# Kernel tuning notes

Hardware: AMD Instinct MI355X
Metric: run time of the kernel (lower is better)

Reference implementation:

```python
import jax, jax.numpy as jnp
import numpy as np

B, N, D, H, P = 4, 512, 256, 8, 3
HD = D // H
EPS = 1e-5

def _ln(x, g, b):
    m = jnp.mean(x, axis=-1, keepdims=True)
    v = jnp.var(x, axis=-1, keepdims=True)
    return (x - m) * jax.lax.rsqrt(v + EPS) * g + b

def setup_inputs() -> dict:
    key = jax.random.key(0)
    ks = jax.random.split(key, 12)
    s = lambda *sh: 1.0 / np.sqrt(sh[0])
    return {
        "x": jax.random.normal(ks[0], (B, N, D), jnp.float32),
        "mask": jax.random.randint(ks[1], (B, N), 0, 2).astype(bool),
        "pair_feat": jax.random.normal(ks[2], (B, N, N, P), jnp.float32),
        "Wqkv": jax.random.normal(ks[3], (D, 3 * D), jnp.float32) * s(D),
        "Wout": jax.random.normal(ks[4], (D, D), jnp.float32) * s(D),
        "bout": jnp.zeros((D,), jnp.float32),
        "Wp1": jax.random.normal(ks[5], (P, D), jnp.float32) * s(P),
        "bp1": jnp.zeros((D,), jnp.float32),
        "Wp2": jax.random.normal(ks[6], (D, H), jnp.float32) * s(D),
        "bp2": jnp.zeros((H,), jnp.float32),
        "Wf1": jax.random.normal(ks[7], (D, 4 * D), jnp.float32) * s(D),
        "bf1": jnp.zeros((4 * D,), jnp.float32),
        "Wf2": jax.random.normal(ks[8], (4 * D, D), jnp.float32) * s(4 * D),
        "bf2": jnp.zeros((D,), jnp.float32),
        "g1": jnp.ones((D,), jnp.float32), "b1": jnp.zeros((D,), jnp.float32),
        "g2": jnp.ones((D,), jnp.float32), "b2": jnp.zeros((D,), jnp.float32),
    }

def reference(x, mask, pair_feat, Wqkv, Wout, bout, Wp1, bp1, Wp2, bp2,
              Wf1, bf1, Wf2, bf2, g1, b1, g2, b2):
    b_, n_, d_ = x.shape
    scale = HD ** -0.5
    qkv = x @ Wqkv                                  # [B,N,3D]
    q, k, v = jnp.split(qkv, 3, axis=-1)
    q = q.reshape(b_, n_, H, HD)
    k = k.reshape(b_, n_, H, HD)
    v = v.reshape(b_, n_, H, HD)
    logits = jnp.einsum('bihd,bjhd->bhij', q, k) * scale
    # pairwise bias MLP -> per-head bias [B,H,N,N]
    bias = jax.nn.relu(pair_feat @ Wp1 + bp1) @ Wp2 + bp2   # [B,N,N,H]
    logits = logits + jnp.transpose(bias, (0, 3, 1, 2))
    key_mask = ~mask[:, None, None, :]               # [B,1,1,N]
    logits = jnp.where(key_mask, -1e9, logits)
    attn = jax.nn.softmax(logits, axis=-1)
    out = jnp.einsum('bhij,bjhd->bihd', attn, v).reshape(b_, n_, d_)
    out = out @ Wout + bout
    x = _ln(x + out, g1, b1)
    h = jax.nn.gelu(x @ Wf1 + bf1, approximate=False) @ Wf2 + bf2
    return _ln(x + h, g2, b2)
```

## Files before the change

kernel.cpp:

```cpp
#include <hip/hip_runtime.h>
#include <hip/hip_fp16.h>
#include <math.h>

typedef unsigned short u16;
typedef short s16x8 __attribute__((ext_vector_type(8)));
typedef _Float16 f16x8 __attribute__((ext_vector_type(8)));
typedef float f32x4 __attribute__((ext_vector_type(4)));
typedef unsigned int u32x2 __attribute__((ext_vector_type(2)));

constexpr int CB = 4, CN = 512, CD = 256, CH = 8, CHD = 32;
constexpr float CEPS = 1e-5f;
constexpr int M_ROWS = CB * CN;
constexpr float QSCALE = 0.17677669529663687f;

constexpr size_t O_XB    = 0;
constexpr size_t O_QB    = 1048576;
constexpr size_t O_KB    = 2097152;
constexpr size_t O_VT    = 3145728;
constexpr size_t O_WQKVT = 4194304;
constexpr size_t O_WOUTT = O_WQKVT + 393216;
constexpr size_t O_WF1T  = O_WOUTT + 131072;
constexpr size_t O_WF2T  = O_WF1T + 524288;
constexpr size_t O_WP2T  = O_WF2T + 524288;
constexpr size_t O_PACKED= O_WP2T + 8192;
constexpr size_t O_MASKD = O_PACKED + 4096;
constexpr size_t O_BIAS  = O_MASKD + 8192;
constexpr size_t O_AOUT  = O_BIAS + 16777216;
constexpr size_t O_X1F   = O_AOUT + 1048576;
constexpr size_t O_X1B   = O_X1F + 2097152;
constexpr size_t O_H1B   = O_X1B + 1048576;
constexpr size_t O_PRE1  = O_H1B + 4194304;
constexpr size_t O_PRE2  = O_PRE1 + 2097152;

__device__ inline u16 f2b(float f) {
  union { float f; unsigned u; } v{f};
  return (u16)((v.u + 0x7FFFu + ((v.u >> 16) & 1u)) >> 16);
}
__device__ inline float b2f(u16 b) {
  union { unsigned u; float f; } v{(unsigned)b << 16};
  return v.f;
}
__device__ inline f32x4 MFMA(s16x8 a, s16x8 b, f32x4 c) {
  return __builtin_amdgcn_mfma_f32_16x16x32_bf16(a, b, c, 0, 0, 0);
}
__device__ inline f32x4 MFMAH(f16x8 a, f16x8 b, f32x4 c) {
  return __builtin_amdgcn_mfma_f32_16x16x32_f16(a, b, c, 0, 0, 0);
}
__device__ inline unsigned cvtpk(float lo, float hi) {
  unsigned r;
  asm("v_cvt_pk_bf16_f32 %0, %1, %2" : "=v"(r) : "v"(lo), "v"(hi));
  return r;
}
__device__ inline unsigned pkmax0(unsigned a) {
  unsigned d;
  asm("v_pk_max_f16 %0, %1, 0" : "=v"(d) : "v"(a));
  return d;
}

__global__ __launch_bounds__(256) void prep_kernel(
    const float* __restrict__ x, const float* __restrict__ Wqkv,
    const float* __restrict__ Wout, const float* __restrict__ Wf1,
    const float* __restrict__ Wf2, const float* __restrict__ Wp2,
    const float* __restrict__ Wp1, const float* __restrict__ bp1,
    const unsigned char* __restrict__ maskraw,
    u16* __restrict__ xb, u16* __restrict__ wqkvt, u16* __restrict__ woutt,
    u16* __restrict__ wf1t, u16* __restrict__ wf2t, u16* __restrict__ wp2t,
    unsigned* __restrict__ packed, int* __restrict__ maskd) {
  __shared__ int mode_max;
  int blk = blockIdx.x, tid = threadIdx.x;
  if (blk < 256) {
    for (int t = tid; t < 512; t += 256) {
      float4 v = ((const float4*)x)[blk * 512 + t];
      u16 o0 = f2b(v.x), o1 = f2b(v.y), o2 = f2b(v.z), o3 = f2b(v.w);
      u32x2 w; w.x = (unsigned)o0 | ((unsigned)o1 << 16);
      w.y = (unsigned)o2 | ((unsigned)o3 << 16);
      *(u32x2*)(xb + (size_t)(blk * 512 + t) * 4) = w;
    }
  } else if (blk < 352) {
    int o0 = (blk - 256) * 2048;
    for (int t = tid; t < 2048; t += 256) {
      int o = o0 + t, n = o >> 8, k = o & 255;
      wqkvt[o] = f2b(Wqkv[k * 768 + n]);
    }
  } else if (blk < 384) {
    int o0 = (blk - 352) * 2048;
    for (int t = tid; t < 2048; t += 256) {
      int o = o0 + t, n = o >> 8, k = o & 255;
      woutt[o] = f2b(Wout[k * 256 + n]);
    }
  } else if (blk < 512) {
    int o0 = (blk - 384) * 2048;
    for (int t = tid; t < 2048; t += 256) {
      int o = o0 + t, n = o >> 8, k = o & 255;
      wf1t[o] = f2b(Wf1[k * 1024 + n]);
    }
  } else if (blk < 640) {
    int o0 = (blk - 512) * 2048;
    for (int t = tid; t < 2048; t += 256) {
      int o = o0 + t, n = o >> 10, k = o & 1023;
      wf2t[o] = f2b(Wf2[k * 256 + n]);
    }
  } else if (blk == 640) {
    for (int t = tid; t < 4096; t += 256) {
      int h = t >> 8, c = t & 255;
      wp2t[t] = (h < 8) ? __half_as_ushort(__float2half(Wp2[c * 8 + h])) : (u16)0;
    }
    if (tid < 128) {
      int p = tid * 2;
      unsigned w0 = (unsigned)__half_as_ushort(__float2half(Wp1[p]))
                  | ((unsigned)__half_as_ushort(__float2half(Wp1[p + 1])) << 16);
      unsigned w1 = (unsigned)__half_as_ushort(__float2half(Wp1[256 + p]))
                  | ((unsigned)__half_as_ushort(__float2half(Wp1[256 + p + 1])) << 16);
      unsigned w2 = (unsigned)__half_as_ushort(__float2half(Wp1[512 + p]))
                  | ((unsigned)__half_as_ushort(__float2half(Wp1[512 + p + 1])) << 16);
      unsigned bb = (unsigned)__half_as_ushort(__float2half(bp1[p]))
                  | ((unsigned)__half_as_ushort(__float2half(bp1[p + 1])) << 16);
      uint4 o; o.x = w0; o.y = w1; o.z = w2; o.w = bb;
      ((uint4*)packed)[tid] = o;
    }
  } else {
    if (tid == 0) mode_max = 0;
    __syncthreads();
    int lm = 0;
    for (int i = tid; i < CB*CN; i += 256)
      if ((i & 3) != 0) lm = max(lm, (int)maskraw[i]);
    atomicMax(&mode_max, lm);
    __syncthreads();
    int mv = mode_max;
    for (int i = tid; i < CB*CN; i += 256) {
      int val;
      if (mv == 0)      val = (((const int*)maskraw)[i] != 0);
      else if (mv == 1) val = (maskraw[i] != 0);
      else              val = (((const unsigned int*)maskraw)[i] != 0);
      maskd[i] = val;
    }
  }
}

template<int EPI, int BM>
__global__ __launch_bounds__(256) void mgemm(
    const u16* __restrict__ A, const u16* __restrict__ Wt,
    const float* __restrict__ bias, const float* __restrict__ R,
    float* __restrict__ outf, u16* __restrict__ outb,
    u16* __restrict__ qb, u16* __restrict__ kb, u16* __restrict__ vt,
    int M, int N, int K) {
  constexpr int MF = BM / 32;
  __shared__ u16 As[BM * 64];
  __shared__ u16 Bs[64 * 64];
  const int tid = threadIdx.x;
  const int lane = tid & 63, w = tid >> 6;
  const int wm = w >> 1, wn = w & 1;
  const int bm = blockIdx.y * BM, bn = blockIdx.x * 64;
  f32x4 fz = {0.f, 0.f, 0.f, 0.f};
  f32x4 acc[MF][2];
#pragma unroll
  for (int mf = 0; mf < MF; ++mf) { acc[mf][0] = fz; acc[mf][1] = fz; }
  for (int k0 = 0; k0 < K; k0 += 64) {
#pragma unroll
    for (int t = tid; t < BM * 8; t += 256) {
      int r = t >> 3, s = t & 7;
      s16x8 v = *(const s16x8*)(A + (size_t)(bm + r) * K + k0 + s * 8);
      *(s16x8*)(As + r * 64 + ((s ^ (r & 7)) << 3)) = v;
    }
#pragma unroll
    for (int t = tid; t < 512; t += 256) {
      int r = t >> 3, s = t & 7;
      s16x8 v = *(const s16x8*)(Wt + (size_t)(bn + r) * K + k0 + s * 8);
      *(s16x8*)(Bs + r * 64 + ((s ^ (r & 7)) << 3)) = v;
    }
    __syncthreads();
#pragma unroll
    for (int ks = 0; ks < 2; ++ks) {
      s16x8 af[MF], bf[2];
#pragma unroll
      for (int mf = 0; mf < MF; ++mf) {
        int r = wm * (16 * MF) + mf * 16 + (lane & 15);
        int s = ks * 4 + (lane >> 4);
        af[mf] = *(const s16x8*)(As + r * 64 + ((s ^ (r & 7)) << 3));
      }
#pragma unroll
      for (int nf = 0; nf < 2; ++nf) {
        int r = wn * 32 + nf * 16 + (lane & 15);
        int s = ks * 4 + (lane >> 4);
        bf[nf] = *(const s16x8*)(Bs + r * 64 + ((s ^ (r & 7)) << 3));
      }
#pragma unroll
      for (int mf = 0; mf < MF; ++mf)
#pragma unroll
        for (int nf = 0; nf < 2; ++nf)
          acc[mf][nf] = MFMA(af[mf], bf[nf], acc[mf][nf]);
    }
    __syncthreads();
  }
#pragma unroll
  for (int mf = 0; mf < MF; ++mf) {
#pragma unroll
    for (int nf = 0; nf < 2; ++nf) {
#pragma unroll
      for (int r = 0; r < 4; ++r) {
        int m = bm + wm * (16 * MF) + mf * 16 + (lane >> 4) * 4 + r;
        int n = bn + wn * 32 + nf * 16 + (lane & 15);
        float v = acc[mf][nf][r];
        if (EPI == 0) {
          if (n < 256) {
            qb[(size_t)m * 256 + n] = f2b(v * QSCALE);
          } else if (n < 512) {
            kb[(size_t)m * 256 + (n - 256)] = f2b(v);
          } else {
            int nv = n - 512, h = nv >> 5, d = nv & 31;
            int bb = m >> 9, j = m & 511;
            vt[(size_t)((bb * 8 + h) * 32 + d) * 512 + j] = f2b(v);
          }
        } else if (EPI == 1) {
          outf[(size_t)m * N + n] = v + bias[n] + R[(size_t)m * N + n];
        } else {
          float g = v + bias[n];
          g = 0.5f * g * (1.0f + erff(g * 0.70710678118654752f));
          outb[(size_t)m * N + n] = f2b(g);
        }
      }
    }
  }
}

__global__ __launch_bounds__(256) void pbias_kernel(
    const float* __restrict__ pf, const unsigned* __restrict__ packed,
    const u16* __restrict__ wp2t, const float* __restrict__ bp2,
    u16* __restrict__ biasout) {
  const int bid = blockIdx.x;
  const int b = bid >> 9, i = bid & 511;
  const int tid = threadIdx.x;
  const int lane = tid & 63, w = tid >> 6;
  const int q = lane >> 4, hr = lane & 15;
  __shared__ uint4 pk[128];
  if (tid < 128) pk[tid] = ((const uint4*)packed)[tid];
  const float* pfb = pf + (size_t)(b * 512 + i) * 1536;
  __half2 f0d[8], f1d[8], f2d[8];
#pragma unroll
  for (int t = 0; t < 8; ++t) {
    int j = w * 128 + t * 16 + hr;
    f0d[t] = __float2half2_rn(pfb[j * 3 + 0]);
    f1d[t] = __float2half2_rn(pfb[j * 3 + 1]);
    f2d[t] = __float2half2_rn(pfb[j * 3 + 2]);
  }
  __syncthreads();
  f32x4 fz = {0.f, 0.f, 0.f, 0.f};
  f32x4 acc[8] = {fz, fz, fz, fz, fz, fz, fz, fz};
  for (int chunk = 0; chunk < 8; ++chunk) {
    f16x8 wfrag = *(const f16x8*)(wp2t + hr * 256 + chunk * 32 + q * 8);
    int pbase = chunk * 16 + q * 4;
    __half2 w0[4], w1[4], w2[4], bb[4];
#pragma unroll
    for (int p = 0; p < 4; ++p) {
      uint4 c = pk[pbase + p];
      w0[p] = *(const __half2*)&c.x;
      w1[p] = *(const __half2*)&c.y;
      w2[p] = *(const __half2*)&c.z;
      bb[p] = *(const __half2*)&c.w;
    }
#pragma unroll
    for (int t = 0; t < 8; ++t) {
      union { unsigned u[4]; f16x8 v; } af;
#pragma unroll
      for (int p = 0; p < 4; ++p) {
        __half2 h = __hfma2(f0d[t], w0[p], bb[p]);
        h = __hfma2(f1d[t], w1[p], h);
        h = __hfma2(f2d[t], w2[p], h);
        af.u[p] = pkmax0(*(const unsigned*)&h);
      }
      acc[t] = MFMAH(af.v, wfrag, acc[t]);
    }
  }
  if (hr < 8) {
    float bb = bp2[hr];
    size_t base = ((size_t)(b * 8 + hr) * 512 + i) * 512;
#pragma unroll
    for (int t = 0; t < 8; ++t) {
      int j0 = w * 128 + t * 16 + q * 4;
      u32x2 o;
      o.x = cvtpk(acc[t][0] + bb, acc[t][1] + bb);
      o.y = cvtpk(acc[t][2] + bb, acc[t][3] + bb);
      *(u32x2*)(biasout + base + j0) = o;
    }
  }
}

__global__ __launch_bounds__(512) void flash_kernel(
    const u16* __restrict__ qb, const u16* __restrict__ kb,
    const u16* __restrict__ vt, const u16* __restrict__ biasin,
    const int* __restrict__ maskd, u16* __restrict__ aout) {
  const int i0 = blockIdx.x * 64, h = blockIdx.y, b = blockIdx.z;
  const int tid = threadIdx.x;
  const int lane = tid & 63, w = tid >> 6;
  const int mf = w & 3, jhalf = w >> 2;
  __shared__ u16 qs[64 * 32];
  __shared__ u16 ksh[128 * 32];
  __shared__ u16 vs[32 * 128];
  __shared__ u16 bs[64 * 128];
  __shared__ u16 ps[8][16 * 64];
  __shared__ float cmb[4][2][16][2];
  for (int t = tid; t < 256; t += 512) {
    int r = t >> 2, s = t & 3;
    s16x8 v = *(const s16x8*)(qb + (size_t)(b * 512 + i0 + r) * 256 + h * 32 + s * 8);
    *(s16x8*)(qs + r * 32 + ((s ^ (r & 3)) << 3)) = v;
  }
  f32x4 fz = {0.f, 0.f, 0.f, 0.f};
  f32x4 oacc[2] = {fz, fz};
  float mrun[4] = {-3e38f, -3e38f, -3e38f, -3e38f};
  float lrun[4] = {0.f, 0.f, 0.f, 0.f};
  const int* mrow = maskd + b * 512;
  const int jj0 = jhalf * 64;
  for (int jc = 0; jc < 4; ++jc) {
    int j0 = jc * 128;
    for (int t = tid; t < 512; t += 512) {
      int r = t >> 2, s = t & 3;
      s16x8 v = *(const s16x8*)(kb + (size_t)(b * 512 + j0 + r) * 256 + h * 32 + s * 8);
      *(s16x8*)(ksh + r * 32 + ((s ^ (r & 3)) << 3)) = v;
    }
    for (int t = tid; t < 512; t += 512) {
      int r = t >> 4, s = t & 15;
      s16x8 v = *(const s16x8*)(vt + (size_t)((b * 8 + h) * 32 + r) * 512 + j0 + s * 8);
      *(s16x8*)(vs + r * 128 + (((s & 8) | ((s & 7) ^ (r & 7))) << 3)) = v;
    }
#pragma unroll
    for (int t = tid; t < 1024; t += 512) {
      int r = t >> 4, s = t & 15;
      s16x8 v = *(const s16x8*)(biasin + ((size_t)((b * 8 + h) * 512 + i0 + r)) * 512 + j0 + s * 8);
      *(s16x8*)(bs + r * 128 + (((s & 8) | ((s & 7) ^ (r & 7))) << 3)) = v;
    }
    __syncthreads();
    int mk[4];
#pragma unroll
    for (int jf = 0; jf < 4; ++jf)
      mk[jf] = mrow[j0 + jj0 + jf * 16 + (lane & 15)];
    int arow = mf * 16 + (lane & 15);
    s16x8 af = *(const s16x8*)(qs + arow * 32 + (((lane >> 4) ^ (arow & 3)) << 3));
    f32x4 sm[4];
#pragma unroll
    for (int jf = 0; jf < 4; ++jf) {
      int brow = jj0 + jf * 16 + (lane & 15);
      s16x8 bfr = *(const s16x8*)(ksh + brow * 32 + (((lane >> 4) ^ (brow & 3)) << 3));
      sm[jf] = MFMA(af, bfr, fz);
    }
    int il = mf * 16 + (lane >> 4) * 4;
#pragma unroll
    for (int jf = 0; jf < 4; ++jf) {
#pragma unroll
      for (int r = 0; r < 4; ++r) {
        int i_loc = il + r;
        int jb = jj0 + jf * 16 + (lane & 15);
        int slot = jb >> 3;
        float bv = b2f(bs[i_loc * 128 + (((slot & 8) | ((slot & 7) ^ (i_loc & 7))) << 3) + (jb & 7)]);
        float sval = sm[jf][r] + bv;
        sm[jf][r] = mk[jf] ? sval : -1e9f;
      }
    }
    float mx[4];
#pragma unroll
    for (int r = 0; r < 4; ++r)
      mx[r] = fmaxf(fmaxf(sm[0][r], sm[1][r]), fmaxf(sm[2][r], sm[3][r]));
#pragma unroll
    for (int d = 1; d < 16; d <<= 1)
#pragma unroll
      for (int r = 0; r < 4; ++r) mx[r] = fmaxf(mx[r], __shfl_xor(mx[r], d));
    float psl[4] = {0.f, 0.f, 0.f, 0.f};
#pragma unroll
    for (int jf = 0; jf < 4; ++jf)
#pragma unroll
      for (int r = 0; r < 4; ++r) {
        float p = __expf(sm[jf][r] - mx[r]);
        sm[jf][r] = p; psl[r] += p;
      }
#pragma unroll
    for (int d = 1; d < 16; d <<= 1)
#pragma unroll
      for (int r = 0; r < 4; ++r) psl[r] += __shfl_xor(psl[r], d);
    if ((lane & 15) == 0) {
#pragma unroll
      for (int r = 0; r < 4; ++r) {
        int row = (lane >> 4) * 4 + r;
        cmb[mf][jhalf][row][0] = mx[r];
        cmb[mf][jhalf][row][1] = psl[r];
      }
    }
    __syncthreads();
    float selfs[4];
#pragma unroll
    for (int r = 0; r < 4; ++r) {
      int row = (lane >> 4) * 4 + r;
      float omx = cmb[mf][1 - jhalf][row][0];
      float ops = cmb[mf][1 - jhalf][row][1];
      float tm = fmaxf(mx[r], omx);
      float nm = fmaxf(mrun[r], tm);
      float sc = __expf(mrun[r] - nm);
      selfs[r] = __expf(mx[r] - nm);
      float ptile = psl[r] * selfs[r] + ops * __expf(omx - nm);
      lrun[r] = lrun[r] * sc + ptile;
      mrun[r] = nm;
      oacc[0][r] *= sc; oacc[1][r] *= sc;
    }
    u16* pw = &ps[w][0];
#pragma unroll
    for (int jf = 0; jf < 4; ++jf) {
      int jcol = jf * 16 + (lane & 15);
      int slot = jcol >> 3, el = jcol & 7;
#pragma unroll
      for (int r = 0; r < 4; ++r) {
        int row = (lane >> 4) * 4 + r;
        pw[row * 64 + ((slot ^ (row & 7)) << 3) + el] = f2b(sm[jf][r] * selfs[r]);
      }
    }
#pragma unroll
    for (int kw = 0; kw < 2; ++kw) {
      int prow = lane & 15;
      s16x8 pa = *(const s16x8*)(pw + prow * 64 + (((kw * 4 + (lane >> 4)) ^ (prow & 7)) << 3));
#pragma unroll
      for (int df = 0; df < 2; ++df) {
        int drow = df * 16 + (lane & 15);
        int jcol = jj0 + kw * 32 + ((lane >> 4) << 3);
        int slot = jcol >> 3;
        s16x8 vb = *(const s16x8*)(vs + drow * 128 + (((slot & 8) | ((slot & 7) ^ (drow & 7))) << 3));
        oacc[df] = MFMA(pa, vb, oacc[df]);
      }
    }
    __syncthreads();
  }
  float* obuf = (float*)bs;
  if (jhalf == 1) {
#pragma unroll
    for (int r = 0; r < 4; ++r) {
      int row = mf * 16 + (lane >> 4) * 4 + r;
#pragma unroll
      for (int df = 0; df < 2; ++df)
        obuf[row * 33 + df * 16 + (lane & 15)] = oacc[df][r];
    }
  }
  __syncthreads();
  if (jhalf == 0) {
#pragma unroll
    for (int r = 0; r < 4; ++r) {
      float inv = 1.0f / lrun[r];
      int row = mf * 16 + (lane >> 4) * 4 + r;
      int i = i0 + row;
#pragma unroll
      for (int df = 0; df < 2; ++df) {
        int d = df * 16 + (lane & 15);
        float o = (oacc[df][r] + obuf[row * 33 + d]) * inv;
        aout[(size_t)(b * 512 + i) * 256 + h * 32 + d] = f2b(o);
      }
    }
  }
}

template<bool WB>
__global__ __launch_bounds__(256) void ln_kernel(
    const float* __restrict__ in, const float* __restrict__ g,
    const float* __restrict__ be, float* __restrict__ op,
    u16* __restrict__ ob) {
  int row = blockIdx.x * 4 + (threadIdx.x >> 6);
  int lane = threadIdx.x & 63;
  const float* x = in + (size_t)row * CD;
  float4 v = *(const float4*)&x[lane * 4];
  float s  = v.x + v.y + v.z + v.w;
  float ss = v.x*v.x + v.y*v.y + v.z*v.z + v.w*v.w;
#pragma unroll
  for (int off = 32; off > 0; off >>= 1) {
    s  += __shfl_xor(s, off);
    ss += __shfl_xor(ss, off);
  }
  float mean = s * (1.0f / CD);
  float var  = ss * (1.0f / CD) - mean * mean;
  float inv  = rsqrtf(var + CEPS);
  float4 gg = *(const float4*)&g[lane * 4];
  float4 bb = *(const float4*)&be[lane * 4];
  float4 o;
  o.x = (v.x - mean) * inv * gg.x + bb.x;
  o.y = (v.y - mean) * inv * gg.y + bb.y;
  o.z = (v.z - mean) * inv * gg.z + bb.z;
  o.w = (v.w - mean) * inv * gg.w + bb.w;
  *(float4*)&op[(size_t)row * CD + lane * 4] = o;
  if (WB) {
    u32x2 w; w.x = (unsigned)f2b(o.x) | ((unsigned)f2b(o.y) << 16);
    w.y = (unsigned)f2b(o.z) | ((unsigned)f2b(o.w) << 16);
    *(u32x2*)(ob + (size_t)row * CD + lane * 4) = w;
  }
}

extern "C" void kernel_launch(void* const* d_in, const int* in_sizes, int n_in,
                              void* d_out, int out_size, void* d_ws, size_t ws_size,
                              hipStream_t stream) {
  (void)in_sizes; (void)n_in; (void)out_size; (void)ws_size;
  const float* x    = (const float*)d_in[0];
  const void*  mask = d_in[1];
  const float* pf   = (const float*)d_in[2];
  const float* Wqkv = (const float*)d_in[3];
  const float* Wout = (const float*)d_in[4];
  const float* bout = (const float*)d_in[5];
  const float* Wp1  = (const float*)d_in[6];
  const float* bp1  = (const float*)d_in[7];
  const float* Wp2  = (const float*)d_in[8];
  const float* bp2  = (const float*)d_in[9];
  const float* Wf1  = (const float*)d_in[10];
  const float* bf1  = (const float*)d_in[11];
  const float* Wf2  = (const float*)d_in[12];
  const float* bf2  = (const float*)d_in[13];
  const float* g1   = (const float*)d_in[14];
  const float* b1   = (const float*)d_in[15];
  const float* g2   = (const float*)d_in[16];
  const float* b2   = (const float*)d_in[17];

  char* ws = (char*)d_ws;
  u16* xb     = (u16*)(ws + O_XB);
  u16* qb     = (u16*)(ws + O_QB);
  u16* kb     = (u16*)(ws + O_KB);
  u16* vt     = (u16*)(ws + O_VT);
  u16* wqkvt  = (u16*)(ws + O_WQKVT);
  u16* woutt  = (u16*)(ws + O_WOUTT);
  u16* wf1t   = (u16*)(ws + O_WF1T);
  u16* wf2t   = (u16*)(ws + O_WF2T);
  u16* wp2t   = (u16*)(ws + O_WP2T);
  unsigned* packed = (unsigned*)(ws + O_PACKED);
  int* maskd  = (int*)(ws + O_MASKD);
  u16* biasb  = (u16*)(ws + O_BIAS);
  u16* aout   = (u16*)(ws + O_AOUT);
  float* x1f  = (float*)(ws + O_X1F);
  u16* x1b    = (u16*)(ws + O_X1B);
  u16* h1b    = (u16*)(ws + O_H1B);
  float* pre1 = (float*)(ws + O_PRE1);
  float* pre2 = (float*)(ws + O_PRE2);
  float* out  = (float*)d_out;

  hipLaunchKernelGGL(prep_kernel, dim3(642), dim3(256), 0, stream,
                     x, Wqkv, Wout, Wf1, Wf2, Wp2, Wp1, bp1,
                     (const unsigned char*)mask,
                     xb, wqkvt, woutt, wf1t, wf2t, wp2t, packed, maskd);
  hipLaunchKernelGGL((mgemm<0, 64>), dim3(12, 32), dim3(256), 0, stream,
                     xb, wqkvt, nullptr, nullptr, nullptr, nullptr,
                     qb, kb, vt, M_ROWS, 768, 256);
  hipLaunchKernelGGL(pbias_kernel, dim3(2048), dim3(256), 0, stream,
                     pf, packed, wp2t, bp2, biasb);
  hipLaunchKernelGGL(flash_kernel, dim3(8, 8, 4), dim3(512), 0, stream,
                     qb, kb, vt, biasb, maskd, aout);
  hipLaunchKernelGGL((mgemm<1, 32>), dim3(4, 64), dim3(256), 0, stream,
                     aout, woutt, bout, x, pre1, nullptr,
                     nullptr, nullptr, nullptr, M_ROWS, 256, 256);
  hipLaunchKernelGGL((ln_kernel<true>), dim3(M_ROWS / 4), dim3(256), 0, stream,
                     pre1, g1, b1, x1f, x1b);
  hipLaunchKernelGGL((mgemm<2, 64>), dim3(16, 32), dim3(256), 0, stream,
                     x1b, wf1t, bf1, nullptr, nullptr, h1b,
                     nullptr, nullptr, nullptr, M_ROWS, 1024, 256);
  hipLaunchKernelGGL((mgemm<1, 32>), dim3(4, 64), dim3(256), 0, stream,
                     h1b, wf2t, bf2, x1f, pre2, nullptr,
                     nullptr, nullptr, nullptr, M_ROWS, 256, 1024);
  hipLaunchKernelGGL((ln_kernel<false>), dim3(M_ROWS / 4), dim3(256), 0, stream,
                     pre2, g2, b2, out, nullptr);
}
```

Before: 104.1 us.

## Merge QKV GEMM with pair-bias kernel and fold LayerNorm1 into FFN GEMMs

The QKV projection and the pairwise-bias MLP now run as a single launch, with the block index choosing which branch a block executes. This removes one launch and lets the two independent workloads share the GPU. The first LayerNorm kernel is removed: the FFN1 GEMM recomputes row statistics from pre1 and normalises while loading its A tile, and the FFN2 epilogue recomputes the normalised residual. This drops the x1f and x1b intermediate buffers and a launch, at the cost of redundant statistic computation in every FFN block and more global reads of pre1.

```diff
diff --git a/kernel.cpp b/kernel.cpp
--- a/kernel.cpp
+++ b/kernel.cpp
@@ -26,9 +26,7 @@
 constexpr size_t O_MASKD = O_PACKED + 4096;
 constexpr size_t O_BIAS  = O_MASKD + 8192;
 constexpr size_t O_AOUT  = O_BIAS + 16777216;
-constexpr size_t O_X1F   = O_AOUT + 1048576;
-constexpr size_t O_X1B   = O_X1F + 2097152;
-constexpr size_t O_H1B   = O_X1B + 1048576;
+constexpr size_t O_H1B   = O_AOUT + 1048576;
 constexpr size_t O_PRE1  = O_H1B + 4194304;
 constexpr size_t O_PRE2  = O_PRE1 + 2097152;
 
@@ -137,71 +135,68 @@
   }
 }
 
-template<int EPI, int BM>
-__global__ __launch_bounds__(256) void mgemm(
+__global__ __launch_bounds__(256) void qkv_pbias_kernel(
     const u16* __restrict__ A, const u16* __restrict__ Wt,
-    const float* __restrict__ bias, const float* __restrict__ R,
-    float* __restrict__ outf, u16* __restrict__ outb,
     u16* __restrict__ qb, u16* __restrict__ kb, u16* __restrict__ vt,
-    int M, int N, int K) {
-  constexpr int MF = BM / 32;
-  __shared__ u16 As[BM * 64];
-  __shared__ u16 Bs[64 * 64];
-  const int tid = threadIdx.x;
+    const float* __restrict__ pf, const unsigned* __restrict__ packed,
+    const u16* __restrict__ wp2t, const float* __restrict__ bp2,
+    u16* __restrict__ biasout) {
+  __shared__ uint4 smem[1024];
+  const int blk = blockIdx.x, tid = threadIdx.x;
   const int lane = tid & 63, w = tid >> 6;
-  const int wm = w >> 1, wn = w & 1;
-  const int bm = blockIdx.y * BM, bn = blockIdx.x * 64;
-  f32x4 fz = {0.f, 0.f, 0.f, 0.f};
-  f32x4 acc[MF][2];
-#pragma unroll
-  for (int mf = 0; mf < MF; ++mf) { acc[mf][0] = fz; acc[mf][1] = fz; }
-  for (int k0 = 0; k0 < K; k0 += 64) {
-#pragma unroll
-    for (int t = tid; t < BM * 8; t += 256) {
-      int r = t >> 3, s = t & 7;
-      s16x8 v = *(const s16x8*)(A + (size_t)(bm + r) * K + k0 + s * 8);
-      *(s16x8*)(As + r * 64 + ((s ^ (r & 7)) << 3)) = v;
-    }
-#pragma unroll
-    for (int t = tid; t < 512; t += 256) {
-      int r = t >> 3, s = t & 7;
-      s16x8 v = *(const s16x8*)(Wt + (size_t)(bn + r) * K + k0 + s * 8);
-      *(s16x8*)(Bs + r * 64 + ((s ^ (r & 7)) << 3)) = v;
-    }
-    __syncthreads();
-#pragma unroll
-    for (int ks = 0; ks < 2; ++ks) {
-      s16x8 af[MF], bf[2];
-#pragma unroll
-      for (int mf = 0; mf < MF; ++mf) {
-        int r = wm * (16 * MF) + mf * 16 + (lane & 15);
-        int s = ks * 4 + (lane >> 4);
-        af[mf] = *(const s16x8*)(As + r * 64 + ((s ^ (r & 7)) << 3));
-      }
+  if (blk < 384) {
+    u16* As = (u16*)smem;
+    u16* Bs = (u16*)smem + 64 * 64;
+    const int wm = w >> 1, wn = w & 1;
+    const int bm = (blk / 12) * 64, bn = (blk % 12) * 64;
+    f32x4 fz = {0.f, 0.f, 0.f, 0.f};
+    f32x4 acc[2][2] = {{fz, fz}, {fz, fz}};
+    for (int k0 = 0; k0 < 256; k0 += 64) {
+#pragma unroll
+      for (int t = tid; t < 512; t += 256) {
+        int r = t >> 3, s = t & 7;
+        s16x8 v = *(const s16x8*)(A + (size_t)(bm + r) * 256 + k0 + s * 8);
+        *(s16x8*)(As + r * 64 + ((s ^ (r & 7)) << 3)) = v;
+      }
+#pragma unroll
+      for (int t = tid; t < 512; t += 256) {
+        int r = t >> 3, s = t & 7;
+        s16x8 v = *(const s16x8*)(Wt + (size_t)(bn + r) * 256 + k0 + s * 8);
+        *(s16x8*)(Bs + r * 64 + ((s ^ (r & 7)) << 3)) = v;
+      }
+      __syncthreads();
+#pragma unroll
+      for (int ks = 0; ks < 2; ++ks) {
+        s16x8 af[2], bf[2];
+#pragma unroll
+        for (int mf = 0; mf < 2; ++mf) {
+          int r = wm * 32 + mf * 16 + (lane & 15);
+          int s = ks * 4 + (lane >> 4);
+          af[mf] = *(const s16x8*)(As + r * 64 + ((s ^ (r & 7)) << 3));
+        }
+#pragma unroll
+        for (int nf = 0; nf < 2; ++nf) {
+          int r = wn * 32 + nf * 16 + (lane & 15);
+          int s = ks * 4 + (lane >> 4);
+          bf[nf] = *(const s16x8*)(Bs + r * 64 + ((s ^ (r & 7)) << 3));
+        }
+#pragma unroll
+        for (int mf = 0; mf < 2; ++mf)
+#pragma unroll
+          for (int nf = 0; nf < 2; ++nf)
+            acc[mf][nf] = MFMA(af[mf], bf[nf], acc[mf][nf]);
+      }
+      __syncthreads();
+    }
+#pragma unroll
+    for (int mf = 0; mf < 2; ++mf) {
 #pragma unroll
       for (int nf = 0; nf < 2; ++nf) {
-        int r = wn * 32 + nf * 16 + (lane & 15);
-        int s = ks * 4 + (lane >> 4);
-        bf[nf] = *(const s16x8*)(Bs + r * 64 + ((s ^ (r & 7)) << 3));
-      }
-#pragma unroll
-      for (int mf = 0; mf < MF; ++mf)
-#pragma unroll
-        for (int nf = 0; nf < 2; ++nf)
-          acc[mf][nf] = MFMA(af[mf], bf[nf], acc[mf][nf]);
-    }
-    __syncthreads();
-  }
-#pragma unroll
-  for (int mf = 0; mf < MF; ++mf) {
-#pragma unroll
-    for (int nf = 0; nf < 2; ++nf) {
-#pragma unroll
-      for (int r = 0; r < 4; ++r) {
-        int m = bm + wm * (16 * MF) + mf * 16 + (lane >> 4) * 4 + r;
-        int n = bn + wn * 32 + nf * 16 + (lane & 15);
-        float v = acc[mf][nf][r];
-        if (EPI == 0) {
+#pragma unroll
+        for (int r = 0; r < 4; ++r) {
+          int m = bm + wm * 32 + mf * 16 + (lane >> 4) * 4 + r;
+          int n = bn + wn * 32 + nf * 16 + (lane & 15);
+          float v = acc[mf][nf][r];
           if (n < 256) {
             qb[(size_t)m * 256 + n] = f2b(v * QSCALE);
           } else if (n < 512) {
@@ -211,76 +206,282 @@
             int bb = m >> 9, j = m & 511;
             vt[(size_t)((bb * 8 + h) * 32 + d) * 512 + j] = f2b(v);
           }
-        } else if (EPI == 1) {
-          outf[(size_t)m * N + n] = v + bias[n] + R[(size_t)m * N + n];
-        } else {
-          float g = v + bias[n];
-          g = 0.5f * g * (1.0f + erff(g * 0.70710678118654752f));
-          outb[(size_t)m * N + n] = f2b(g);
         }
       }
     }
-  }
-}
-
-__global__ __launch_bounds__(256) void pbias_kernel(
-    const float* __restrict__ pf, const unsigned* __restrict__ packed,
-    const u16* __restrict__ wp2t, const float* __restrict__ bp2,
-    u16* __restrict__ biasout) {
-  const int bid = blockIdx.x;
-  const int b = bid >> 9, i = bid & 511;
+  } else {
+    uint4* pk = smem;
+    const int bid = blk - 384;
+    const int b = bid >> 9, i = bid & 511;
+    const int q = lane >> 4, hr = lane & 15;
+    if (tid < 128) pk[tid] = ((const uint4*)packed)[tid];
+    const float* pfb = pf + (size_t)(b * 512 + i) * 1536;
+    __half2 f0d[8], f1d[8], f2d[8];
+#pragma unroll
+    for (int t = 0; t < 8; ++t) {
+      int j = w * 128 + t * 16 + hr;
+      f0d[t] = __float2half2_rn(pfb[j * 3 + 0]);
+      f1d[t] = __float2half2_rn(pfb[j * 3 + 1]);
+      f2d[t] = __float2half2_rn(pfb[j * 3 + 2]);
+    }
+    __syncthreads();
+    f32x4 fz = {0.f, 0.f, 0.f, 0.f};
+    f32x4 acc[8] = {fz, fz, fz, fz, fz, fz, fz, fz};
+    for (int chunk = 0; chunk < 8; ++chunk) {
+      f16x8 wfrag = *(const f16x8*)(wp2t + hr * 256 + chunk * 32 + q * 8);
+      int pbase = chunk * 16 + q * 4;
+      __half2 w0[4], w1[4], w2[4], bb[4];
+#pragma unroll
+      for (int p = 0; p < 4; ++p) {
+        uint4 c = pk[pbase + p];
+        w0[p] = *(const __half2*)&c.x;
+        w1[p] = *(const __half2*)&c.y;
+        w2[p] = *(const __half2*)&c.z;
+        bb[p] = *(const __half2*)&c.w;
+      }
+#pragma unroll
+      for (int t = 0; t < 8; ++t) {
+        union { unsigned u[4]; f16x8 v; } af;
+#pragma unroll
+        for (int p = 0; p < 4; ++p) {
+          __half2 h = __hfma2(f0d[t], w0[p], bb[p]);
+          h = __hfma2(f1d[t], w1[p], h);
+          h = __hfma2(f2d[t], w2[p], h);
+          af.u[p] = pkmax0(*(const unsigned*)&h);
+        }
+        acc[t] = MFMAH(af.v, wfrag, acc[t]);
+      }
+    }
+    if (hr < 8) {
+      float bb = bp2[hr];
+      size_t base = ((size_t)(b * 8 + hr) * 512 + i) * 512;
+#pragma unroll
+      for (int t = 0; t < 8; ++t) {
+        int j0 = w * 128 + t * 16 + q * 4;
+        u32x2 o;
+        o.x = cvtpk(acc[t][0] + bb, acc[t][1] + bb);
+        o.y = cvtpk(acc[t][2] + bb, acc[t][3] + bb);
+        *(u32x2*)(biasout + base + j0) = o;
+      }
+    }
+  }
+}
+
+__global__ __launch_bounds__(256) void mgemm_res(
+    const u16* __restrict__ A, const u16* __restrict__ Wt,
+    const float* __restrict__ bias, const float* __restrict__ R,
+    float* __restrict__ outf, int N, int K) {
+  __shared__ u16 As[32 * 64];
+  __shared__ u16 Bs[64 * 64];
   const int tid = threadIdx.x;
   const int lane = tid & 63, w = tid >> 6;
-  const int q = lane >> 4, hr = lane & 15;
-  __shared__ uint4 pk[128];
-  if (tid < 128) pk[tid] = ((const uint4*)packed)[tid];
-  const float* pfb = pf + (size_t)(b * 512 + i) * 1536;
-  __half2 f0d[8], f1d[8], f2d[8];
-#pragma unroll
-  for (int t = 0; t < 8; ++t) {
-    int j = w * 128 + t * 16 + hr;
-    f0d[t] = __float2half2_rn(pfb[j * 3 + 0]);
-    f1d[t] = __float2half2_rn(pfb[j * 3 + 1]);
-    f2d[t] = __float2half2_rn(pfb[j * 3 + 2]);
+  const int wm = w >> 1, wn = w & 1;
+  const int bm = blockIdx.y * 32, bn = blockIdx.x * 64;
+  f32x4 fz = {0.f, 0.f, 0.f, 0.f};
+  f32x4 acc[2] = {fz, fz};
+  for (int k0 = 0; k0 < K; k0 += 64) {
+    for (int t = tid; t < 256; t += 256) {
+      int r = t >> 3, s = t & 7;
+      s16x8 v = *(const s16x8*)(A + (size_t)(bm + r) * K + k0 + s * 8);
+      *(s16x8*)(As + r * 64 + ((s ^ (r & 7)) << 3)) = v;
+    }
+#pragma unroll
+    for (int t = tid; t < 512; t += 256) {
+      int r = t >> 3, s = t & 7;
+      s16x8 v = *(const s16x8*)(Wt + (size_t)(bn + r) * K + k0 + s * 8);
+      *(s16x8*)(Bs + r * 64 + ((s ^ (r & 7)) << 3)) = v;
+    }
+    __syncthreads();
+#pragma unroll
+    for (int ks = 0; ks < 2; ++ks) {
+      int r = wm * 16 + (lane & 15);
+      int s = ks * 4 + (lane >> 4);
+      s16x8 af = *(const s16x8*)(As + r * 64 + ((s ^ (r & 7)) << 3));
+#pragma unroll
+      for (int nf = 0; nf < 2; ++nf) {
+        int br = wn * 32 + nf * 16 + (lane & 15);
+        s16x8 bf = *(const s16x8*)(Bs + br * 64 + ((s ^ (br & 7)) << 3));
+        acc[nf] = MFMA(af, bf, acc[nf]);
+      }
+    }
+    __syncthreads();
+  }
+#pragma unroll
+  for (int nf = 0; nf < 2; ++nf) {
+#pragma unroll
+    for (int r = 0; r < 4; ++r) {
+      int m = bm + wm * 16 + (lane >> 4) * 4 + r;
+      int n = bn + wn * 32 + nf * 16 + (lane & 15);
+      outf[(size_t)m * N + n] = acc[nf][r] + bias[n] + R[(size_t)m * N + n];
+    }
+  }
+}
+
+__global__ __launch_bounds__(256) void ffn1_kernel(
+    const float* __restrict__ pre1, const u16* __restrict__ Wt,
+    const float* __restrict__ bias, const float* __restrict__ g1,
+    const float* __restrict__ b1, u16* __restrict__ outb) {
+  __shared__ u16 As[64 * 64];
+  __shared__ u16 Bs[64 * 64];
+  __shared__ float rowm[64], rowr[64];
+  const int tid = threadIdx.x;
+  const int lane = tid & 63, w = tid >> 6;
+  const int wm = w >> 1, wn = w & 1;
+  const int bm = blockIdx.y * 64, bn = blockIdx.x * 64;
+  {
+    int r = tid >> 2, qd = tid & 3;
+    const float4* pr = (const float4*)(pre1 + (size_t)(bm + r) * 256 + qd * 64);
+    float s = 0.f, ss = 0.f;
+#pragma unroll
+    for (int u = 0; u < 16; ++u) {
+      float4 v = pr[u];
+      s += v.x + v.y + v.z + v.w;
+      ss += v.x*v.x + v.y*v.y + v.z*v.z + v.w*v.w;
+    }
+    s += __shfl_xor(s, 1); ss += __shfl_xor(ss, 1);
+    s += __shfl_xor(s, 2); ss += __shfl_xor(ss, 2);
+    if (qd == 0) {
+      float mean = s * (1.0f / 256.0f);
+      float var  = ss * (1.0f / 256.0f) - mean * mean;
+      rowm[r] = mean; rowr[r] = rsqrtf(var + CEPS);
+    }
   }
   __syncthreads();
   f32x4 fz = {0.f, 0.f, 0.f, 0.f};
-  f32x4 acc[8] = {fz, fz, fz, fz, fz, fz, fz, fz};
-  for (int chunk = 0; chunk < 8; ++chunk) {
-    f16x8 wfrag = *(const f16x8*)(wp2t + hr * 256 + chunk * 32 + q * 8);
-    int pbase = chunk * 16 + q * 4;
-    __half2 w0[4], w1[4], w2[4], bb[4];
-#pragma unroll
-    for (int p = 0; p < 4; ++p) {
-      uint4 c = pk[pbase + p];
-      w0[p] = *(const __half2*)&c.x;
-      w1[p] = *(const __half2*)&c.y;
-      w2[p] = *(const __half2*)&c.z;
-      bb[p] = *(const __half2*)&c.w;
-    }
-#pragma unroll
-    for (int t = 0; t < 8; ++t) {
-      union { unsigned u[4]; f16x8 v; } af;
-#pragma unroll
-      for (int p = 0; p < 4; ++p) {
-        __half2 h = __hfma2(f0d[t], w0[p], bb[p]);
-        h = __hfma2(f1d[t], w1[p], h);
-        h = __hfma2(f2d[t], w2[p], h);
-        af.u[p] = pkmax0(*(const unsigned*)&h);
-      }
-      acc[t] = MFMAH(af.v, wfrag, acc[t]);
-    }
-  }
-  if (hr < 8) {
-    float bb = bp2[hr];
-    size_t base = ((size_t)(b * 8 + hr) * 512 + i) * 512;
-#pragma unroll
-    for (int t = 0; t < 8; ++t) {
-      int j0 = w * 128 + t * 16 + q * 4;
-      u32x2 o;
-      o.x = cvtpk(acc[t][0] + bb, acc[t][1] + bb);
-      o.y = cvtpk(acc[t][2] + bb, acc[t][3] + bb);
-      *(u32x2*)(biasout + base + j0) = o;
+  f32x4 acc[2][2] = {{fz, fz}, {fz, fz}};
+  for (int k0 = 0; k0 < 256; k0 += 64) {
+#pragma unroll
+    for (int t = tid; t < 512; t += 256) {
+      int r = t >> 3, s = t & 7;
+      float mean = rowm[r], rstd = rowr[r];
+      const float4* pr = (const float4*)(pre1 + (size_t)(bm + r) * 256 + k0 + s * 8);
+      float4 a0 = pr[0], a1 = pr[1];
+      const float4* gp = (const float4*)(g1 + k0 + s * 8);
+      const float4* bp = (const float4*)(b1 + k0 + s * 8);
+      float4 g0 = gp[0], g1v = gp[1], c0 = bp[0], c1 = bp[1];
+      union { unsigned u[4]; s16x8 v; } pk2;
+      pk2.u[0] = cvtpk((a0.x-mean)*rstd*g0.x + c0.x, (a0.y-mean)*rstd*g0.y + c0.y);
+      pk2.u[1] = cvtpk((a0.z-mean)*rstd*g0.z + c0.z, (a0.w-mean)*rstd*g0.w + c0.w);
+      pk2.u[2] = cvtpk((a1.x-mean)*rstd*g1v.x + c1.x, (a1.y-mean)*rstd*g1v.y + c1.y);
+      pk2.u[3] = cvtpk((a1.z-mean)*rstd*g1v.z + c1.z, (a1.w-mean)*rstd*g1v.w + c1.w);
+      *(s16x8*)(As + r * 64 + ((s ^ (r & 7)) << 3)) = pk2.v;
+    }
+#pragma unroll
+    for (int t = tid; t < 512; t += 256) {
+      int r = t >> 3, s = t & 7;
+      s16x8 v = *(const s16x8*)(Wt + (size_t)(bn + r) * 256 + k0 + s * 8);
+      *(s16x8*)(Bs + r * 64 + ((s ^ (r & 7)) << 3)) = v;
+    }
+    __syncthreads();
+#pragma unroll
+    for (int ks = 0; ks < 2; ++ks) {
+      s16x8 af[2], bf[2];
+#pragma unroll
+      for (int mf = 0; mf < 2; ++mf) {
+        int r = wm * 32 + mf * 16 + (lane & 15);
+        int s = ks * 4 + (lane >> 4);
+        af[mf] = *(const s16x8*)(As + r * 64 + ((s ^ (r & 7)) << 3));
+      }
+#pragma unroll
+      for (int nf = 0; nf < 2; ++nf) {
+        int r = wn * 32 + nf * 16 + (lane & 15);
+        int s = ks * 4 + (lane >> 4);
+        bf[nf] = *(const s16x8*)(Bs + r * 64 + ((s ^ (r & 7)) << 3));
+      }
+#pragma unroll
+      for (int mf = 0; mf < 2; ++mf)
+#pragma unroll
+        for (int nf = 0; nf < 2; ++nf)
+          acc[mf][nf] = MFMA(af[mf], bf[nf], acc[mf][nf]);
+    }
+    __syncthreads();
+  }
+#pragma unroll
+  for (int mf = 0; mf < 2; ++mf) {
+#pragma unroll
+    for (int nf = 0; nf < 2; ++nf) {
+#pragma unroll
+      for (int r = 0; r < 4; ++r) {
+        int m = bm + wm * 32 + mf * 16 + (lane >> 4) * 4 + r;
+        int n = bn + wn * 32 + nf * 16 + (lane & 15);
+        float gv = acc[mf][nf][r] + bias[n];
+        gv = 0.5f * gv * (1.0f + erff(gv * 0.70710678118654752f));
+        outb[(size_t)m * 1024 + n] = f2b(gv);
+      }
+    }
+  }
+}
+
+__global__ __launch_bounds__(256) void ffn2_kernel(
+    const u16* __restrict__ A, const u16* __restrict__ Wt,
+    const float* __restrict__ bias, const float* __restrict__ pre1,
+    const float* __restrict__ g1, const float* __restrict__ b1,
+    float* __restrict__ outf) {
+  __shared__ u16 As[32 * 64];
+  __shared__ u16 Bs[64 * 64];
+  __shared__ float rowm[32], rowr[32];
+  const int tid = threadIdx.x;
+  const int lane = tid & 63, w = tid >> 6;
+  const int wm = w >> 1, wn = w & 1;
+  const int bm = blockIdx.y * 32, bn = blockIdx.x * 64;
+  {
+    int r = tid >> 3, od = tid & 7;
+    const float4* pr = (const float4*)(pre1 + (size_t)(bm + r) * 256 + od * 32);
+    float s = 0.f, ss = 0.f;
+#pragma unroll
+    for (int u = 0; u < 8; ++u) {
+      float4 v = pr[u];
+      s += v.x + v.y + v.z + v.w;
+      ss += v.x*v.x + v.y*v.y + v.z*v.z + v.w*v.w;
+    }
+    s += __shfl_xor(s, 1); ss += __shfl_xor(ss, 1);
+    s += __shfl_xor(s, 2); ss += __shfl_xor(ss, 2);
+    s += __shfl_xor(s, 4); ss += __shfl_xor(ss, 4);
+    if (od == 0) {
+      float mean = s * (1.0f / 256.0f);
+      float var  = ss * (1.0f / 256.0f) - mean * mean;
+      rowm[r] = mean; rowr[r] = rsqrtf(var + CEPS);
+    }
+  }
+  __syncthreads();
+  f32x4 fz = {0.f, 0.f, 0.f, 0.f};
+  f32x4 acc[2] = {fz, fz};
+  for (int k0 = 0; k0 < 1024; k0 += 64) {
+    for (int t = tid; t < 256; t += 256) {
+      int r = t >> 3, s = t & 7;
+      s16x8 v = *(const s16x8*)(A + (size_t)(bm + r) * 1024 + k0 + s * 8);
+      *(s16x8*)(As + r * 64 + ((s ^ (r & 7)) << 3)) = v;
+    }
+#pragma unroll
+    for (int t = tid; t < 512; t += 256) {
+      int r = t >> 3, s = t & 7;
+      s16x8 v = *(const s16x8*)(Wt + (size_t)(bn + r) * 1024 + k0 + s * 8);
+      *(s16x8*)(Bs + r * 64 + ((s ^ (r & 7)) << 3)) = v;
+    }
+    __syncthreads();
+#pragma unroll
+    for (int ks = 0; ks < 2; ++ks) {
+      int r = wm * 16 + (lane & 15);
+      int s = ks * 4 + (lane >> 4);
+      s16x8 af = *(const s16x8*)(As + r * 64 + ((s ^ (r & 7)) << 3));
+#pragma unroll
+      for (int nf = 0; nf < 2; ++nf) {
+        int br = wn * 32 + nf * 16 + (lane & 15);
+        s16x8 bf = *(const s16x8*)(Bs + br * 64 + ((s ^ (br & 7)) << 3));
+        acc[nf] = MFMA(af, bf, acc[nf]);
+      }
+    }
+    __syncthreads();
+  }
+#pragma unroll
+  for (int nf = 0; nf < 2; ++nf) {
+#pragma unroll
+    for (int r = 0; r < 4; ++r) {
+      int m = bm + wm * 16 + (lane >> 4) * 4 + r;
+      int n = bn + wn * 32 + nf * 16 + (lane & 15);
+      float mean = rowm[m - bm], rstd = rowr[m - bm];
+      float xr = (pre1[(size_t)m * 256 + n] - mean) * rstd * g1[n] + b1[n];
+      outf[(size_t)m * 256 + n] = acc[nf][r] + bias[n] + xr;
     }
   }
 }
@@ -452,11 +653,9 @@
   }
 }
 
-template<bool WB>
 __global__ __launch_bounds__(256) void ln_kernel(
     const float* __restrict__ in, const float* __restrict__ g,
-    const float* __restrict__ be, float* __restrict__ op,
-    u16* __restrict__ ob) {
+    const float* __restrict__ be, float* __restrict__ op) {
   int row = blockIdx.x * 4 + (threadIdx.x >> 6);
   int lane = threadIdx.x & 63;
   const float* x = in + (size_t)row * CD;
@@ -479,11 +678,6 @@
   o.z = (v.z - mean) * inv * gg.z + bb.z;
   o.w = (v.w - mean) * inv * gg.w + bb.w;
   *(float4*)&op[(size_t)row * CD + lane * 4] = o;
-  if (WB) {
-    u32x2 w; w.x = (unsigned)f2b(o.x) | ((unsigned)f2b(o.y) << 16);
-    w.y = (unsigned)f2b(o.z) | ((unsigned)f2b(o.w) << 16);
-    *(u32x2*)(ob + (size_t)row * CD + lane * 4) = w;
-  }
 }
 
 extern "C" void kernel_launch(void* const* d_in, const int* in_sizes, int n_in,
@@ -523,8 +717,6 @@
   int* maskd  = (int*)(ws + O_MASKD);
   u16* biasb  = (u16*)(ws + O_BIAS);
   u16* aout   = (u16*)(ws + O_AOUT);
-  float* x1f  = (float*)(ws + O_X1F);
-  u16* x1b    = (u16*)(ws + O_X1B);
   u16* h1b    = (u16*)(ws + O_H1B);
   float* pre1 = (float*)(ws + O_PRE1);
   float* pre2 = (float*)(ws + O_PRE2);
@@ -534,24 +726,17 @@
                      x, Wqkv, Wout, Wf1, Wf2, Wp2, Wp1, bp1,
                      (const unsigned char*)mask,
                      xb, wqkvt, woutt, wf1t, wf2t, wp2t, packed, maskd);
-  hipLaunchKernelGGL((mgemm<0, 64>), dim3(12, 32), dim3(256), 0, stream,
-                     xb, wqkvt, nullptr, nullptr, nullptr, nullptr,
-                     qb, kb, vt, M_ROWS, 768, 256);
-  hipLaunchKernelGGL(pbias_kernel, dim3(2048), dim3(256), 0, stream,
+  hipLaunchKernelGGL(qkv_pbias_kernel, dim3(2432), dim3(256), 0, stream,
+                     xb, wqkvt, qb, kb, vt,
                      pf, packed, wp2t, bp2, biasb);
   hipLaunchKernelGGL(flash_kernel, dim3(8, 8, 4), dim3(512), 0, stream,
                      qb, kb, vt, biasb, maskd, aout);
-  hipLaunchKernelGGL((mgemm<1, 32>), dim3(4, 64), dim3(256), 0, stream,
-                     aout, woutt, bout, x, pre1, nullptr,
-                     nullptr, nullptr, nullptr, M_ROWS, 256, 256);
-  hipLaunchKernelGGL((ln_kernel<true>), dim3(M_ROWS / 4), dim3(256), 0, stream,
-                     pre1, g1, b1, x1f, x1b);
-  hipLaunchKernelGGL((mgemm<2, 64>), dim3(16, 32), dim3(256), 0, stream,
-                     x1b, wf1t, bf1, nullptr, nullptr, h1b,
-                     nullptr, nullptr, nullptr, M_ROWS, 1024, 256);
-  hipLaunchKernelGGL((mgemm<1, 32>), dim3(4, 64), dim3(256), 0, stream,
-                     h1b, wf2t, bf2, x1f, pre2, nullptr,
-                     nullptr, nullptr, nullptr, M_ROWS, 256, 1024);
-  hipLaunchKernelGGL((ln_kernel<false>), dim3(M_ROWS / 4), dim3(256), 0, stream,
-                     pre2, g2, b2, out, nullptr);
-}
+  hipLaunchKernelGGL(mgemm_res, dim3(4, 64), dim3(256), 0, stream,
+                     aout, woutt, bout, x, pre1, 256, 256);
+  hipLaunchKernelGGL(ffn1_kernel, dim3(16, 32), dim3(256), 0, stream,
+                     pre1, wf1t, bf1, g1, b1, h1b);
+  hipLaunchKernelGGL(ffn2_kernel, dim3(4, 64), dim3(256), 0, stream,
+                     h1b, wf2t, bf2, pre1, g1, b1, pre2);
+  hipLaunchKernelGGL(ln_kernel, dim3(M_ROWS / 4), dim3(256), 0, stream,
+                     pre2, g2, b2, out);
+}
```

Result: faster. 99.90 us (-4.0%).
